# Performance work log

Hardware: AMD Instinct MI355X
Metric: run time of the kernel (lower is better)

Reference implementation:

```python
import jax, jax.numpy as jnp
import numpy as np
import math
from jax import lax

D = 256      # d_model
H = 8        # heads
DK = D // H  # 32
P = 16       # patch size
IMG = 224
S = (IMG // P) ** 2 + 1  # 197
B = 64
EPS = 1e-5


def _ln(x, g, b):
    m = jnp.mean(x, axis=-1, keepdims=True)
    v = jnp.mean((x - m) ** 2, axis=-1, keepdims=True)
    return (x - m) / jnp.sqrt(v + EPS) * g + b


def _attn(q_in, k_in, v_in, wq, bq, wk, bk, wv, bv, wo, bo, mask):
    # torch Linear: y = x @ W^T + b
    def heads(x, w, b):
        y = x @ w.T + b
        bsz, s, _ = y.shape
        return y.reshape(bsz, s, H, DK).transpose(0, 2, 1, 3)  # [b,h,s,dk]
    q = heads(q_in, wq, bq)
    k = heads(k_in, wk, bk)
    v = heads(v_in, wv, bv)
    att = jnp.einsum('bhqd,bhkd->bhqk', q, k) / math.sqrt(DK)
    if mask is not None:
        att = jnp.where(mask == 0, -jnp.inf, att)
    att = jax.nn.softmax(att, axis=-1)
    o = jnp.einsum('bhqk,bhkd->bhqd', att, v)
    bsz, s, _ = q_in.shape  # output reshape uses q's shape (faithful to source)
    o = o.transpose(0, 2, 1, 3).reshape(bsz, s, D)
    return o @ wo.T + bo


def _patch_embed(img, conv_w, conv_b, cls, pos):
    x = lax.conv_general_dilated(img, conv_w, window_strides=(P, P),
                                 padding='VALID',
                                 dimension_numbers=('NCHW', 'OIHW', 'NCHW'))
    x = x + conv_b[None, :, None, None]
    bsz = img.shape[0]
    x = x.reshape(bsz, D, -1).transpose(0, 2, 1)  # [B,196,D]
    cls_t = jnp.broadcast_to(cls, (bsz, 1, D))
    x = jnp.concatenate([x, cls_t], axis=1)  # cls appended at END (faithful)
    return x + pos


def setup_inputs() -> dict:
    key = jax.random.key(0)
    ks = iter(jax.random.split(key, 64))
    nrm = lambda shape, s=0.02: jax.random.normal(next(ks), shape, jnp.float32) * s
    inp = {
        'enc_out': jax.random.normal(next(ks), (B, 3, IMG, IMG), jnp.float32),
        'dec_in': jax.random.normal(next(ks), (B, S, D), jnp.float32),
        'mask': jnp.ones((1, 1, S, S), jnp.int32),
        'conv_w': nrm((D, 3, P, P)),
        'conv_b': jnp.zeros((D,), jnp.float32),
        'cls': nrm((1, 1, D), 1.0),
        'pos': nrm((1, S, D), 1.0),
        'ff_w1': nrm((4 * D, D)), 'ff_b1': jnp.zeros((4 * D,), jnp.float32),
        'ff_w2': nrm((D, 4 * D)), 'ff_b2': jnp.zeros((D,), jnp.float32),
        'ln1_g': jnp.ones((D,), jnp.float32), 'ln1_b': jnp.zeros((D,), jnp.float32),
        'ln2_g': jnp.ones((D,), jnp.float32), 'ln2_b': jnp.zeros((D,), jnp.float32),
        'ln3_g': jnp.ones((D,), jnp.float32), 'ln3_b': jnp.zeros((D,), jnp.float32),
    }
    for p in ('a1', 'a2'):
        for n in ('wq', 'wk', 'wv', 'wo'):
            inp[f'{p}_{n}'] = nrm((D, D))
            inp[f'{p}_b{n[1]}'] = jnp.zeros((D,), jnp.float32)
    return inp


def reference(enc_out, dec_in, mask, conv_w, conv_b, cls, pos,
              ff_w1, ff_b1, ff_w2, ff_b2,
              ln1_g, ln1_b, ln2_g, ln2_b, ln3_g, ln3_b,
              a1_wq, a1_bq, a1_wk, a1_bk, a1_wv, a1_bv, a1_wo, a1_bo,
              a2_wq, a2_bq, a2_wk, a2_bk, a2_wv, a2_bv, a2_wo, a2_bo):
    e = _patch_embed(enc_out, conv_w, conv_b, cls, pos)  # [B,197,D]
    x = dec_in
    x = _ln(x + _attn(dec_in, dec_in, dec_in,
                      a1_wq, a1_bq, a1_wk, a1_bk, a1_wv, a1_bv, a1_wo, a1_bo,
                      None), ln1_g, ln1_b)
    # faithful: q=k=enc_out, v=dec_in, with mask
    x = _ln(x + _attn(e, e, dec_in,
                      a2_wq, a2_bq, a2_wk, a2_bk, a2_wv, a2_bv, a2_wo, a2_bo,
                      mask), ln2_g, ln2_b)
    ff = jax.nn.relu(x @ ff_w1.T + ff_b1) @ ff_w2.T + ff_b2
    x = _ln(x + ff, ln3_g, ln3_b)
    return x
```

## Files before the change

kernel.cpp:

```cpp
#include <hip/hip_runtime.h>
#include <hip/hip_bf16.h>
#include <math.h>

#define DMODEL 256
#define NH 8
#define DKH 32
#define SEQ 197
#define BATCH 64
#define NPAT 196
#define FFDIM 1024
#define KCONV 768
#define EPSLN 1e-5f
#define MROWS (BATCH * SEQ)
#define SP 224

typedef __attribute__((ext_vector_type(8))) short short8;
typedef __attribute__((ext_vector_type(4))) short short4v;
typedef __attribute__((ext_vector_type(4))) float floatx4;

__device__ inline short f2b(float f) {
  unsigned u = __float_as_uint(f);
  unsigned r = (u + 0x7FFFu + ((u >> 16) & 1u)) >> 16;
  return (short)r;
}
__device__ inline float b2f(short s) {
  return __uint_as_float(((unsigned)(unsigned short)s) << 16);
}

typedef const __attribute__((address_space(1))) unsigned int gu32;
typedef __attribute__((address_space(3))) unsigned int lu32;
__device__ __forceinline__ void gl_lds16(const void* g, void* l) {
  __builtin_amdgcn_global_load_lds((gu32*)g, (lu32*)l, 16, 0, 0);
}

__device__ __forceinline__ void gemm64_body(
    char* smem, int bx, int by,
    const short* __restrict__ A, const short* __restrict__ W,
    const float* __restrict__ bias, const short* __restrict__ resb,
    float* __restrict__ outf, short* __restrict__ outb,
    int N, int K, int relu)
{
  short* Al = (short*)smem;
  short* Bl = (short*)(smem + 16384);
  const int t = threadIdx.x;
  const int wave = t >> 6, lane = t & 63;
  const int wm = (wave & 1) * 32, wn = (wave >> 1) * 32;
  const int ml = lane & 15, quad = lane >> 4;
  const int m7 = ml & 7;
  const int m0 = bx * 64, n0 = by * 64;

  const int rs = t >> 3;
  const int cs = (t & 7) ^ (rs & 7);
  const short* gA0 = A + (size_t)(m0 + rs) * K + cs * 8;
  const short* gA1 = A + (size_t)(m0 + rs + 32) * K + cs * 8;
  const short* gB0 = W + (size_t)(n0 + rs) * K + cs * 8;
  const short* gB1 = W + (size_t)(n0 + rs + 32) * K + cs * 8;

  int offA[2][2], offB[2][2];
#pragma unroll
  for (int kk = 0; kk < 2; kk++)
#pragma unroll
    for (int i = 0; i < 2; i++) {
      int ra = wm + i * 16 + ml;
      offA[kk][i] = ra * 64 + (((kk * 4 + quad) ^ m7) * 8);
      int rb = wn + i * 16 + ml;
      offB[kk][i] = rb * 64 + (((kk * 4 + quad) ^ m7) * 8);
    }

  floatx4 z = {0.f, 0.f, 0.f, 0.f};
  floatx4 acc[2][2] = {{z, z}, {z, z}};

  const int niter = K >> 6;
  gl_lds16(gA0, Al + t * 8);
  gl_lds16(gA1, Al + t * 8 + 2048);
  gl_lds16(gB0, Bl + t * 8);
  gl_lds16(gB1, Bl + t * 8 + 2048);
  for (int k = 0; k < niter; k++) {
    int cur = k & 1;
    if (k + 1 < niter) {
      int nb = (cur ^ 1) * 4096;
      int k0 = (k + 1) << 6;
      gl_lds16(gA0 + k0, Al + nb + t * 8);
      gl_lds16(gA1 + k0, Al + nb + t * 8 + 2048);
      gl_lds16(gB0 + k0, Bl + nb + t * 8);
      gl_lds16(gB1 + k0, Bl + nb + t * 8 + 2048);
      __builtin_amdgcn_s_waitcnt(0x0F74);
    } else {
      __builtin_amdgcn_s_waitcnt(0x0F70);
    }
    __asm__ volatile("s_barrier" ::: "memory");
    const short* Ac = Al + cur * 4096;
    const short* Bc = Bl + cur * 4096;
#pragma unroll
    for (int kk = 0; kk < 2; kk++) {
      short8 a0 = *(const short8*)&Ac[offA[kk][0]];
      short8 a1 = *(const short8*)&Ac[offA[kk][1]];
      short8 b0 = *(const short8*)&Bc[offB[kk][0]];
      short8 b1 = *(const short8*)&Bc[offB[kk][1]];
      acc[0][0] = __builtin_amdgcn_mfma_f32_16x16x32_bf16(a0, b0, acc[0][0], 0, 0, 0);
      acc[0][1] = __builtin_amdgcn_mfma_f32_16x16x32_bf16(a0, b1, acc[0][1], 0, 0, 0);
      acc[1][0] = __builtin_amdgcn_mfma_f32_16x16x32_bf16(a1, b0, acc[1][0], 0, 0, 0);
      acc[1][1] = __builtin_amdgcn_mfma_f32_16x16x32_bf16(a1, b1, acc[1][1], 0, 0, 0);
    }
    __asm__ volatile("s_barrier" ::: "memory");
  }
#pragma unroll
  for (int i = 0; i < 2; i++)
#pragma unroll
    for (int j = 0; j < 2; j++)
#pragma unroll
      for (int rr = 0; rr < 4; rr++) {
        int row = m0 + wm + i * 16 + quad * 4 + rr;
        int col = n0 + wn + j * 16 + ml;
        float v = acc[i][j][rr] + bias[col];
        if (resb) v += b2f(resb[(size_t)row * N + col]);
        if (relu) v = fmaxf(v, 0.f);
        if (outf) outf[(size_t)row * N + col] = v;
        if (outb) outb[(size_t)row * N + col] = f2b(v);
      }
}

__device__ __forceinline__ void gemm_full_body(
    char* smem, int bx,
    const short* __restrict__ A, const short* __restrict__ W,
    const float* __restrict__ bias, const short* __restrict__ resb,
    const float* __restrict__ g, const float* __restrict__ bln,
    short* __restrict__ outb, float* __restrict__ outfin, int K)
{
  short* Al = (short*)smem;
  short* Bl = (short*)(smem + 8192);
  const int t = threadIdx.x;
  const int wave = t >> 6, lane = t & 63;
  const int ml = lane & 15, quad = lane >> 4;
  const int m0 = bx * 64;

  const int rs = t >> 2;
  const int cs = (t & 3) ^ ((rs ^ (rs >> 2)) & 3);
  const short* gA = A + (size_t)(m0 + rs) * K + cs * 8;
  const short* gB[4];
#pragma unroll
  for (int j = 0; j < 4; j++)
    gB[j] = W + (size_t)(j * 64 + rs) * K + cs * 8;

  const int sm = (ml ^ (ml >> 2)) & 3;
  const int offA = (wave * 16 + ml) * 32 + ((quad ^ sm) * 8);
  const int offBb = ml * 32 + ((quad ^ sm) * 8);

  floatx4 zv = {0.f, 0.f, 0.f, 0.f};
  floatx4 acc[16];
#pragma unroll
  for (int jj = 0; jj < 16; jj++) acc[jj] = zv;

  const int niter = K >> 5;
  gl_lds16(gA, Al + t * 8);
#pragma unroll
  for (int j = 0; j < 4; j++) gl_lds16(gB[j], Bl + j * 2048 + t * 8);
  for (int k = 0; k < niter; k++) {
    int cur = k & 1;
    if (k + 1 < niter) {
      int k0 = (k + 1) << 5;
      int nbA = (cur ^ 1) * 2048, nbB = (cur ^ 1) * 8192;
      gl_lds16(gA + k0, Al + nbA + t * 8);
#pragma unroll
      for (int j = 0; j < 4; j++) gl_lds16(gB[j] + k0, Bl + nbB + j * 2048 + t * 8);
      __builtin_amdgcn_s_waitcnt(0x0F75);
    } else {
      __builtin_amdgcn_s_waitcnt(0x0F70);
    }
    __asm__ volatile("s_barrier" ::: "memory");
    const short* Ac = Al + cur * 2048;
    const short* Bc = Bl + cur * 8192;
    short8 a = *(const short8*)&Ac[offA];
#pragma unroll
    for (int jj = 0; jj < 16; jj++) {
      short8 b = *(const short8*)&Bc[offBb + jj * 512];
      acc[jj] = __builtin_amdgcn_mfma_f32_16x16x32_bf16(a, b, acc[jj], 0, 0, 0);
    }
    __asm__ volatile("s_barrier" ::: "memory");
  }

  const int rbase = m0 + wave * 16 + quad * 4;
  float bias_r[16], g_r[16], bl_r[16];
#pragma unroll
  for (int jj = 0; jj < 16; jj++) {
    int c = jj * 16 + ml;
    bias_r[jj] = bias[c];
    g_r[jj] = g[c];
    bl_r[jj] = bln[c];
  }
#pragma unroll
  for (int jj = 0; jj < 16; jj++)
#pragma unroll
    for (int rr = 0; rr < 4; rr++)
      acc[jj][rr] += bias_r[jj] + b2f(resb[(size_t)(rbase + rr) * DMODEL + jj * 16 + ml]);
#pragma unroll
  for (int rr = 0; rr < 4; rr++) {
    float s = 0.f;
#pragma unroll
    for (int jj = 0; jj < 16; jj++) s += acc[jj][rr];
    s += __shfl_xor(s, 1); s += __shfl_xor(s, 2);
    s += __shfl_xor(s, 4); s += __shfl_xor(s, 8);
    float mean = s * (1.0f / DMODEL);
    float vs = 0.f;
#pragma unroll
    for (int jj = 0; jj < 16; jj++) {
      float d = acc[jj][rr] - mean;
      vs += d * d;
    }
    vs += __shfl_xor(vs, 1); vs += __shfl_xor(vs, 2);
    vs += __shfl_xor(vs, 4); vs += __shfl_xor(vs, 8);
    float inv = rsqrtf(vs * (1.0f / DMODEL) + EPSLN);
    int row = rbase + rr;
#pragma unroll
    for (int jj = 0; jj < 16; jj++) {
      float o = (acc[jj][rr] - mean) * inv * g_r[jj] + bl_r[jj];
      int col = jj * 16 + ml;
      if (outb) outb[(size_t)row * DMODEL + col] = f2b(o);
      if (outfin) outfin[(size_t)row * DMODEL + col] = o;
    }
  }
}

__device__ __forceinline__ void conv64_body(
    char* smem, int bx, int by,
    const float* __restrict__ img, const short* __restrict__ W,
    const float* __restrict__ cb, const float* __restrict__ pos,
    short* __restrict__ e)
{
  short* Al = (short*)smem;
  short* Bl = (short*)(smem + 8192);
  const int t = threadIdx.x;
  const int wave = t >> 6, lane = t & 63;
  const int wm = (wave & 1) * 32, wn = (wave >> 1) * 32;
  const int ml = lane & 15, quad = lane >> 4;
  const int m7 = ml & 7;
  const int m0 = bx * 64, n0 = by * 64;

  int rA = t >> 3, cg = t & 7;
  int pr_off = cg >> 1;
  int px_off = (cg & 1) * 8;
  int csw = cg ^ (rA & 7);
  const float* baseA[2];
  short* lA[2];
#pragma unroll
  for (int p = 0; p < 2; p++) {
    int m = m0 + rA + p * 32;
    int b = m / NPAT, pp = m - b * NPAT;
    int py = pp / 14, px = pp - py * 14;
    baseA[p] = img + (size_t)b * 3 * 50176 + (size_t)(py * 16) * 224 + px * 16 + px_off;
    lA[p] = &Al[(rA + p * 32) * 64 + csw * 8];
  }
  int rs = t >> 3;
  int cs = (t & 7) ^ (rs & 7);
  const short* gB0 = W + (size_t)(n0 + rs) * KCONV + cs * 8;
  const short* gB1 = W + (size_t)(n0 + rs + 32) * KCONV + cs * 8;

  int offA[2][2], offB[2][2];
#pragma unroll
  for (int kk = 0; kk < 2; kk++)
#pragma unroll
    for (int i = 0; i < 2; i++) {
      int ra = wm + i * 16 + ml;
      offA[kk][i] = ra * 64 + (((kk * 4 + quad) ^ m7) * 8);
      int rb = wn + i * 16 + ml;
      offB[kk][i] = rb * 64 + (((kk * 4 + quad) ^ m7) * 8);
    }

  floatx4 z = {0.f, 0.f, 0.f, 0.f};
  floatx4 acc[2][2] = {{z, z}, {z, z}};

  for (int k0 = 0; k0 < KCONV; k0 += 64) {
    int ch = k0 >> 8;
    int rr0 = (k0 & 255) >> 4;
    __syncthreads();
    gl_lds16(gB0 + k0, Bl + t * 8);
    gl_lds16(gB1 + k0, Bl + t * 8 + 2048);
#pragma unroll
    for (int p = 0; p < 2; p++) {
      const float* ap = baseA[p] + (size_t)ch * 50176 + (rr0 + pr_off) * 224;
      float4 a0 = *(const float4*)ap;
      float4 a1 = *(const float4*)(ap + 4);
      short8 av;
      av[0] = f2b(a0.x); av[1] = f2b(a0.y); av[2] = f2b(a0.z); av[3] = f2b(a0.w);
      av[4] = f2b(a1.x); av[5] = f2b(a1.y); av[6] = f2b(a1.z); av[7] = f2b(a1.w);
      *(short8*)lA[p] = av;
    }
    __builtin_amdgcn_s_waitcnt(0x0F70);
    __syncthreads();
#pragma unroll
    for (int kk = 0; kk < 2; kk++) {
      short8 a0 = *(const short8*)&Al[offA[kk][0]];
      short8 a1 = *(const short8*)&Al[offA[kk][1]];
      short8 b0 = *(const short8*)&Bl[offB[kk][0]];
      short8 b1 = *(const short8*)&Bl[offB[kk][1]];
      acc[0][0] = __builtin_amdgcn_mfma_f32_16x16x32_bf16(a0, b0, acc[0][0], 0, 0, 0);
      acc[0][1] = __builtin_amdgcn_mfma_f32_16x16x32_bf16(a0, b1, acc[0][1], 0, 0, 0);
      acc[1][0] = __builtin_amdgcn_mfma_f32_16x16x32_bf16(a1, b0, acc[1][0], 0, 0, 0);
      acc[1][1] = __builtin_amdgcn_mfma_f32_16x16x32_bf16(a1, b1, acc[1][1], 0, 0, 0);
    }
  }
#pragma unroll
  for (int i = 0; i < 2; i++)
#pragma unroll
    for (int j = 0; j < 2; j++)
#pragma unroll
      for (int rr = 0; rr < 4; rr++) {
        int mrow = m0 + wm + i * 16 + quad * 4 + rr;
        int b2 = mrow / NPAT, p2 = mrow - b2 * NPAT;
        int col = n0 + wn + j * 16 + ml;
        e[((size_t)b2 * SEQ + p2) * DMODEL + col] =
            f2b(acc[i][j][rr] + cb[col] + pos[p2 * DMODEL + col]);
      }
}

__device__ __forceinline__ void attn_body(
    char* smem, int bh,
    const short* __restrict__ qp, int qstr,
    const short* __restrict__ kp, int kstr,
    const short* __restrict__ vp, int vstr,
    const unsigned long long* __restrict__ mbits,
    short* __restrict__ op)
{
  short (*ks)[40] = (short(*)[40])smem;
  short (*vt)[SP + 8] = (short(*)[SP + 8])(smem + 17920);
  short* psw = (short*)(smem + 32768);
  int b = bh >> 3, h = bh & 7;
  int t = threadIdx.x;
  int wave = t >> 6, lane = t & 63;
  int ml = lane & 15, quad = lane >> 4;
  short* ps = psw + wave * 640;

  const short* kb = kp + (size_t)b * SEQ * kstr + h * DKH;
  const short* vb = vp + (size_t)b * SEQ * vstr + h * DKH;
  for (int idx = t; idx < SEQ * 4; idx += 256) {
    int s = idx >> 2, c = (idx & 3) * 8;
    *(short8*)&ks[s][c] = *(const short8*)(kb + (size_t)s * kstr + c);
  }
  for (int idx = t; idx < 1024; idx += 256) {
    int s = ((idx >> 8) << 6) + (idx & 63);
    int c = ((idx >> 6) & 3) * 8;
    if (s < SEQ) {
      short8 v8 = *(const short8*)(vb + (size_t)s * vstr + c);
#pragma unroll
      for (int j = 0; j < 8; j++) vt[c + j][s] = v8[j];
    }
  }
  for (int idx = t; idx < DKH * (SP - SEQ); idx += 256) {
    int d = idx / (SP - SEQ), j = SEQ + idx - d * (SP - SEQ);
    vt[d][j] = 0;
  }
  __syncthreads();

  const float scale = 0.17677669529663687f;
  floatx4 z = {0.f, 0.f, 0.f, 0.f};

  for (int ti = wave; ti < 13; ti += 4) {
    int q0 = ti * 16;
    int qrow = q0 + ml;
    int qc = qrow < SEQ ? qrow : SEQ - 1;
    short8 qf = *(const short8*)(qp + ((size_t)b * SEQ + qc) * qstr + h * DKH + quad * 8);
    const unsigned long long* mrow = mbits + (size_t)qc * 4;

    floatx4 accO0 = z, accO1 = z;
    float mrun = -1e30f, lrun = 0.f;

    for (int st = 0; st < 7; st++) {
      int j0 = st * 32;
      short8 k0 = *(const short8*)&ks[j0 + ml][quad * 8];
      short8 k1 = *(const short8*)&ks[j0 + 16 + ml][quad * 8];
      floatx4 s0 = __builtin_amdgcn_mfma_f32_16x16x32_bf16(k0, qf, z, 0, 0, 0);
      floatx4 s1 = __builtin_amdgcn_mfma_f32_16x16x32_bf16(k1, qf, z, 0, 0, 0);
      unsigned long long mb = mrow[j0 >> 6] >> (j0 & 63);
      float sv[8];
#pragma unroll
      for (int r = 0; r < 4; r++) {
        int jl = quad * 4 + r;
        sv[r]     = ((mb >> jl) & 1ull)        ? s0[r] * scale : -1e38f;
        sv[4 + r] = ((mb >> (16 + jl)) & 1ull) ? s1[r] * scale : -1e38f;
      }
      float tm = sv[0];
#pragma unroll
      for (int i = 1; i < 8; i++) tm = fmaxf(tm, sv[i]);
      tm = fmaxf(tm, __shfl_xor(tm, 16));
      tm = fmaxf(tm, __shfl_xor(tm, 32));
      float nm = fmaxf(mrun, tm);
      float alpha = __expf(mrun - nm);
      float pv[8];
      float psum = 0.f;
#pragma unroll
      for (int i = 0; i < 8; i++) { pv[i] = __expf(sv[i] - nm); psum += pv[i]; }
      psum += __shfl_xor(psum, 16);
      psum += __shfl_xor(psum, 32);
      lrun = lrun * alpha + psum;
      mrun = nm;
      accO0 = accO0 * alpha;
      accO1 = accO1 * alpha;
      short4v p0, p1;
#pragma unroll
      for (int r = 0; r < 4; r++) { p0[r] = f2b(pv[r]); p1[r] = f2b(pv[4 + r]); }
      *(short4v*)&ps[ml * 40 + quad * 4]      = p0;
      *(short4v*)&ps[ml * 40 + 16 + quad * 4] = p1;
      __asm__ volatile("s_waitcnt lgkmcnt(0)" ::: "memory");
      short8 pf = *(const short8*)&ps[ml * 40 + quad * 8];
      short8 vf0 = *(const short8*)&vt[ml][j0 + quad * 8];
      short8 vf1 = *(const short8*)&vt[16 + ml][j0 + quad * 8];
      accO0 = __builtin_amdgcn_mfma_f32_16x16x32_bf16(vf0, pf, accO0, 0, 0, 0);
      accO1 = __builtin_amdgcn_mfma_f32_16x16x32_bf16(vf1, pf, accO1, 0, 0, 0);
    }
    if (qrow < SEQ) {
      float inv = 1.f / lrun;
      short* ob = op + ((size_t)b * SEQ + qrow) * DMODEL + h * DKH;
      short4v o0, o1;
#pragma unroll
      for (int r = 0; r < 4; r++) {
        o0[r] = f2b(accO0[r] * inv);
        o1[r] = f2b(accO1[r] * inv);
      }
      *(short4v*)(ob + quad * 4)      = o0;
      *(short4v*)(ob + 16 + quad * 4) = o1;
    }
  }
}

__global__ __launch_bounds__(256) void phase0(
    const float* wq1, const float* wk1, const float* wv1,
    const float* bq1, const float* bk1, const float* bv1,
    const float* wq2, const float* wk2, const float* bq2, const float* bk2,
    const float* wv2s, const float* wo1, const float* wo2,
    const float* ffw1, const float* ffw2, const float* convw,
    short* Wqkv1, float* Bqkv1, short* Wqk2, float* Bqk2,
    short* Wv2, short* Wo1, short* Wo2, short* Wff1, short* Wff2, short* Wconv,
    const int* mask, unsigned long long* bits, unsigned long long* ones,
    const float* cls, const float* pos, short* e,
    const float* dec, short* dec_bf)
{
  int bid = blockIdx.x;
  int t = threadIdx.x;
  if (bid < 1024) {
    int i = bid * 256 + t;
    if (i < 65536) {
      Wqkv1[i] = f2b(wq1[i]); Wqkv1[65536 + i] = f2b(wk1[i]); Wqkv1[131072 + i] = f2b(wv1[i]);
      Wqk2[i] = f2b(wq2[i]);  Wqk2[65536 + i] = f2b(wk2[i]);
      Wv2[i] = f2b(wv2s[i]);  Wo1[i] = f2b(wo1[i]);  Wo2[i] = f2b(wo2[i]);
    }
    Wff1[i] = f2b(ffw1[i]); Wff2[i] = f2b(ffw2[i]);
    if (i < 196608) Wconv[i] = f2b(convw[i]);
    if (i < 256) {
      Bqkv1[i] = bq1[i]; Bqkv1[256 + i] = bk1[i]; Bqkv1[512 + i] = bv1[i];
      Bqk2[i] = bq2[i];  Bqk2[256 + i] = bk2[i];
    }
  } else if (bid < 1028) {
    int idx = (bid - 1024) * 256 + t;
    if (idx < SEQ * 4) {
      int r = idx >> 2, w = idx & 3;
      unsigned long long bb = 0ull, oo = 0ull;
      for (int j = 0; j < 64; j++) {
        int c = w * 64 + j;
        if (c < SEQ) {
          oo |= (1ull << j);
          if (mask[r * SEQ + c] != 0) bb |= (1ull << j);
        }
      }
      bits[idx] = bb;
      ones[idx] = oo;
    }
  } else if (bid < 1092) {
    int b = bid - 1028, d = t;
    e[((size_t)b * SEQ + NPAT) * DMODEL + d] = f2b(cls[d] + pos[NPAT * DMODEL + d]);
  } else {
    const int ND = (MROWS * DMODEL) / 8;
    int i = (bid - 1092) * 256 + t;
    if (i < ND) {
      float4 a0 = ((const float4*)dec)[i * 2];
      float4 a1 = ((const float4*)dec)[i * 2 + 1];
      short8 o;
      o[0] = f2b(a0.x); o[1] = f2b(a0.y); o[2] = f2b(a0.z); o[3] = f2b(a0.w);
      o[4] = f2b(a1.x); o[5] = f2b(a1.y); o[6] = f2b(a1.z); o[7] = f2b(a1.w);
      ((short8*)dec_bf)[i] = o;
    }
  }
}

__global__ __launch_bounds__(256) void phase1(
    const float* __restrict__ enc, const short* __restrict__ Wconv,
    const float* __restrict__ conv_b, const float* __restrict__ pos,
    short* __restrict__ e_bf,
    const short* __restrict__ dec_bf,
    const short* __restrict__ Wqkv1, const float* __restrict__ Bqkv1,
    short* __restrict__ qkv1,
    const short* __restrict__ Wv2, const float* __restrict__ bv2,
    short* __restrict__ v2)
{
  __shared__ char smem[32768];
  int bid = blockIdx.x;
  if (bid < 784) {
    conv64_body(smem, bid >> 2, bid & 3, enc, Wconv, conv_b, pos, e_bf);
  } else if (bid < 3148) {
    int idx = bid - 784;
    gemm64_body(smem, idx / 12, idx % 12, dec_bf, Wqkv1, Bqkv1, nullptr,
                nullptr, qkv1, 768, 256, 0);
  } else {
    int idx = bid - 3148;
    gemm64_body(smem, idx >> 2, idx & 3, dec_bf, Wv2, bv2, nullptr,
                nullptr, v2, 256, 256, 0);
  }
}

__global__ __launch_bounds__(256) void phase2(
    const short* __restrict__ qkv1, const unsigned long long* __restrict__ mones,
    short* __restrict__ o1,
    const short* __restrict__ e_bf, const short* __restrict__ Wqk2,
    const float* __restrict__ Bqk2, short* __restrict__ qk2)
{
  __shared__ char smem[37888];
  int bid = blockIdx.x;
  if (bid < 512) {
    attn_body(smem, bid, qkv1, 768, qkv1 + 256, 768, qkv1 + 512, 768, mones, o1);
  } else {
    int idx = bid - 512;
    gemm64_body(smem, idx >> 3, idx & 7, e_bf, Wqk2, Bqk2, nullptr,
                nullptr, qk2, 512, 256, 0);
  }
}

__global__ __launch_bounds__(256) void attn_k(
    const short* __restrict__ qp, int qstr,
    const short* __restrict__ kp, int kstr,
    const short* __restrict__ vp, int vstr,
    const unsigned long long* __restrict__ mbits,
    short* __restrict__ op)
{
  __shared__ char smem[37888];
  attn_body(smem, blockIdx.x, qp, qstr, kp, kstr, vp, vstr, mbits, op);
}

__global__ __launch_bounds__(256) void gemm_full_k(
    const short* __restrict__ A, const short* __restrict__ W,
    const float* __restrict__ bias, const short* __restrict__ resb,
    const float* __restrict__ g, const float* __restrict__ bln,
    short* __restrict__ outb, float* __restrict__ outfin, int K)
{
  __shared__ char smem[40960];
  gemm_full_body(smem, blockIdx.x, A, W, bias, resb, g, bln, outb, outfin, K);
}

__global__ __launch_bounds__(256) void gemm_k(
    const short* __restrict__ A, const short* __restrict__ W,
    const float* __restrict__ bias, const short* __restrict__ resb,
    float* __restrict__ outf, short* __restrict__ outb,
    int N, int K, int relu, int nby)
{
  __shared__ char smem[32768];
  gemm64_body(smem, blockIdx.x / nby, blockIdx.x % nby, A, W, bias, resb,
              outf, outb, N, K, relu);
}

extern "C" void kernel_launch(void* const* d_in, const int* in_sizes, int n_in,
                              void* d_out, int out_size, void* d_ws, size_t ws_size,
                              hipStream_t stream)
{
  const float* enc    = (const float*)d_in[0];
  const float* dec_in = (const float*)d_in[1];
  const int*   mask   = (const int*)  d_in[2];
  const float* conv_w = (const float*)d_in[3];
  const float* conv_b = (const float*)d_in[4];
  const float* cls    = (const float*)d_in[5];
  const float* pos    = (const float*)d_in[6];
  const float* ff_w1  = (const float*)d_in[7];
  const float* ff_b1  = (const float*)d_in[8];
  const float* ff_w2  = (const float*)d_in[9];
  const float* ff_b2  = (const float*)d_in[10];
  const float* ln1_g  = (const float*)d_in[11];
  const float* ln1_b  = (const float*)d_in[12];
  const float* ln2_g  = (const float*)d_in[13];
  const float* ln2_b  = (const float*)d_in[14];
  const float* ln3_g  = (const float*)d_in[15];
  const float* ln3_b  = (const float*)d_in[16];
  const float* a1_wq = (const float*)d_in[17]; const float* a1_bq = (const float*)d_in[18];
  const float* a1_wk = (const float*)d_in[19]; const float* a1_bk = (const float*)d_in[20];
  const float* a1_wv = (const float*)d_in[21]; const float* a1_bv = (const float*)d_in[22];
  const float* a1_wo = (const float*)d_in[23]; const float* a1_bo = (const float*)d_in[24];
  const float* a2_wq = (const float*)d_in[25]; const float* a2_bq = (const float*)d_in[26];
  const float* a2_wk = (const float*)d_in[27]; const float* a2_bk = (const float*)d_in[28];
  const float* a2_wv = (const float*)d_in[29]; const float* a2_bv = (const float*)d_in[30];
  const float* a2_wo = (const float*)d_in[31]; const float* a2_bo = (const float*)d_in[32];

  char* wsB = (char*)d_ws;
  short* Wqkv1 = (short*)wsB;
  short* Wqk2  = Wqkv1 + 196608;
  short* Wv2   = Wqk2 + 131072;
  short* Wo1   = Wv2 + 65536;
  short* Wo2   = Wo1 + 65536;
  short* Wff1  = Wo2 + 65536;
  short* Wff2  = Wff1 + 262144;
  short* Wconv = Wff2 + 262144;
  float* Bqkv1 = (float*)(Wconv + 196608);
  float* Bqk2  = Bqkv1 + 768;
  unsigned long long* mbits = (unsigned long long*)(Bqk2 + 512);
  unsigned long long* mones = mbits + 788;

  const size_t MB = 1048576;
  short* dec_bf = (short*)(wsB + 3 * MB);
  short* e_bf   = (short*)(wsB + 10 * MB);
  short* qkv1   = (short*)(wsB + 17 * MB);
  short* o1     = (short*)(wsB + 37 * MB);
  short* qk2    = (short*)(wsB + 44 * MB);
  short* v2     = (short*)(wsB + 57 * MB);
  short* h_buf  = (short*)(wsB + 64 * MB);
  short* x1b    = (short*)(wsB + 97 * MB);
  short* x2b    = (short*)(wsB + 104 * MB);
  short* o2     = o1;

  dim3 blk(256);

  phase0<<<2668, blk, 0, stream>>>(
      a1_wq, a1_wk, a1_wv, a1_bq, a1_bk, a1_bv,
      a2_wq, a2_wk, a2_bq, a2_bk, a2_wv, a1_wo, a2_wo,
      ff_w1, ff_w2, conv_w,
      Wqkv1, Bqkv1, Wqk2, Bqk2, Wv2, Wo1, Wo2, Wff1, Wff2, Wconv,
      mask, mbits, mones, cls, pos, e_bf, dec_in, dec_bf);

  phase1<<<3936, blk, 0, stream>>>(
      enc, Wconv, conv_b, pos, e_bf,
      dec_bf, Wqkv1, Bqkv1, qkv1, Wv2, a2_bv, v2);

  phase2<<<2088, blk, 0, stream>>>(
      qkv1, mones, o1, e_bf, Wqk2, Bqk2, qk2);

  gemm_full_k<<<197, blk, 0, stream>>>(
      o1, Wo1, a1_bo, dec_bf, ln1_g, ln1_b, x1b, nullptr, 256);

  attn_k<<<512, blk, 0, stream>>>(
      qk2, 512, qk2 + 256, 512, v2, 256, mbits, o2);

  gemm_full_k<<<197, blk, 0, stream>>>(
      o2, Wo2, a2_bo, x1b, ln2_g, ln2_b, x2b, nullptr, 256);

  gemm_k<<<3152, blk, 0, stream>>>(
      x2b, Wff1, ff_b1, nullptr, nullptr, h_buf, FFDIM, 256, 1, 16);

  gemm_full_k<<<197, blk, 0, stream>>>(
      h_buf, Wff2, ff_b2, x2b, ln3_g, ln3_b, nullptr, (float*)d_out, 1024);
}
```

Baseline: 326.8 us.

## Keep A row-tile resident in LDS and sweep all output columns per block

Replaces the 64x64 tiled GEMM (grid over M and N tiles) with a row-resident variant: each block loads a 64x256 A tile into LDS once and loops over all N column blocks, streaming only weight slices. The attention-1 QKV and attention-2 V projections are merged into one 1024-wide weight, and the patch-embedding conv computes a full 64x256 output per block. The aim is to avoid re-reading A from global memory for every column tile and to cut block count. In exchange, grids are much smaller (197/393/709 blocks, which may under-fill the GPU), each block runs a long serial loop, and LDS use per block grows.

```diff
diff --git a/kernel.cpp b/kernel.cpp
--- a/kernel.cpp
+++ b/kernel.cpp
@@ -33,91 +33,91 @@
   __builtin_amdgcn_global_load_lds((gu32*)g, (lu32*)l, 16, 0, 0);
 }
 
-__device__ __forceinline__ void gemm64_body(
-    char* smem, int bx, int by,
+__device__ __forceinline__ void gemm_res_body(
+    char* smem, int bx,
     const short* __restrict__ A, const short* __restrict__ W,
-    const float* __restrict__ bias, const short* __restrict__ resb,
-    float* __restrict__ outf, short* __restrict__ outb,
-    int N, int K, int relu)
-{
-  short* Al = (short*)smem;
-  short* Bl = (short*)(smem + 16384);
+    const float* __restrict__ bias,
+    short* __restrict__ outb, int nby, int relu)
+{
+  short* Ar = (short*)smem;
+  short* Bl = (short*)(smem + 33792);
   const int t = threadIdx.x;
   const int wave = t >> 6, lane = t & 63;
   const int wm = (wave & 1) * 32, wn = (wave >> 1) * 32;
   const int ml = lane & 15, quad = lane >> 4;
-  const int m7 = ml & 7;
-  const int m0 = bx * 64, n0 = by * 64;
-
-  const int rs = t >> 3;
-  const int cs = (t & 7) ^ (rs & 7);
-  const short* gA0 = A + (size_t)(m0 + rs) * K + cs * 8;
-  const short* gA1 = A + (size_t)(m0 + rs + 32) * K + cs * 8;
-  const short* gB0 = W + (size_t)(n0 + rs) * K + cs * 8;
-  const short* gB1 = W + (size_t)(n0 + rs + 32) * K + cs * 8;
-
-  int offA[2][2], offB[2][2];
-#pragma unroll
-  for (int kk = 0; kk < 2; kk++)
-#pragma unroll
-    for (int i = 0; i < 2; i++) {
-      int ra = wm + i * 16 + ml;
-      offA[kk][i] = ra * 64 + (((kk * 4 + quad) ^ m7) * 8);
-      int rb = wn + i * 16 + ml;
-      offB[kk][i] = rb * 64 + (((kk * 4 + quad) ^ m7) * 8);
-    }
+  const int m0 = bx * 64;
+  const int Nout = nby * 64;
+
+  {
+    int r = t >> 2, seg = t & 3;
+    const short* gsrc = A + (size_t)(m0 + r) * 256 + seg * 64;
+    short* dst = &Ar[r * 264 + seg * 64];
+#pragma unroll
+    for (int c = 0; c < 8; c++)
+      *(short8*)(dst + c * 8) = *(const short8*)(gsrc + c * 8);
+  }
+  const int rs = t >> 2;
+  const int cs = (t & 3) ^ ((rs ^ (rs >> 2)) & 3);
+  const short* gB = W + (size_t)rs * 256 + cs * 8;
+  short* lB = Bl + t * 8;
+
+  const int rowA0 = (wm + ml) * 264;
+  const int rowA1 = (wm + 16 + ml) * 264;
+  int offB[2];
+#pragma unroll
+  for (int j = 0; j < 2; j++) {
+    int rb = wn + j * 16 + ml;
+    offB[j] = rb * 32 + ((quad ^ ((rb ^ (rb >> 2)) & 3)) * 8);
+  }
+
+  __syncthreads();
 
   floatx4 z = {0.f, 0.f, 0.f, 0.f};
   floatx4 acc[2][2] = {{z, z}, {z, z}};
 
-  const int niter = K >> 6;
-  gl_lds16(gA0, Al + t * 8);
-  gl_lds16(gA1, Al + t * 8 + 2048);
-  gl_lds16(gB0, Bl + t * 8);
-  gl_lds16(gB1, Bl + t * 8 + 2048);
-  for (int k = 0; k < niter; k++) {
-    int cur = k & 1;
-    if (k + 1 < niter) {
-      int nb = (cur ^ 1) * 4096;
-      int k0 = (k + 1) << 6;
-      gl_lds16(gA0 + k0, Al + nb + t * 8);
-      gl_lds16(gA1 + k0, Al + nb + t * 8 + 2048);
-      gl_lds16(gB0 + k0, Bl + nb + t * 8);
-      gl_lds16(gB1 + k0, Bl + nb + t * 8 + 2048);
-      __builtin_amdgcn_s_waitcnt(0x0F74);
+  const int nsteps = nby * 8;
+  gl_lds16(gB, lB);
+  for (int s = 0; s < nsteps; s++) {
+    int by = s >> 3, k = s & 7;
+    if (s + 1 < nsteps) {
+      int by1 = (s + 1) >> 3, k1 = (s + 1) & 7;
+      gl_lds16(gB + (size_t)by1 * (64 * 256) + k1 * 32, lB + ((s + 1) & 1) * 2048);
+      __builtin_amdgcn_s_waitcnt(0x0F71);
     } else {
       __builtin_amdgcn_s_waitcnt(0x0F70);
     }
     __asm__ volatile("s_barrier" ::: "memory");
-    const short* Ac = Al + cur * 4096;
-    const short* Bc = Bl + cur * 4096;
-#pragma unroll
-    for (int kk = 0; kk < 2; kk++) {
-      short8 a0 = *(const short8*)&Ac[offA[kk][0]];
-      short8 a1 = *(const short8*)&Ac[offA[kk][1]];
-      short8 b0 = *(const short8*)&Bc[offB[kk][0]];
-      short8 b1 = *(const short8*)&Bc[offB[kk][1]];
-      acc[0][0] = __builtin_amdgcn_mfma_f32_16x16x32_bf16(a0, b0, acc[0][0], 0, 0, 0);
-      acc[0][1] = __builtin_amdgcn_mfma_f32_16x16x32_bf16(a0, b1, acc[0][1], 0, 0, 0);
-      acc[1][0] = __builtin_amdgcn_mfma_f32_16x16x32_bf16(a1, b0, acc[1][0], 0, 0, 0);
-      acc[1][1] = __builtin_amdgcn_mfma_f32_16x16x32_bf16(a1, b1, acc[1][1], 0, 0, 0);
-    }
+    const short* Bc = Bl + (s & 1) * 2048;
+    int ca = (k * 4 + quad) * 8;
+    short8 a0 = *(const short8*)&Ar[rowA0 + ca];
+    short8 a1 = *(const short8*)&Ar[rowA1 + ca];
+    short8 b0 = *(const short8*)&Bc[offB[0]];
+    short8 b1 = *(const short8*)&Bc[offB[1]];
+    acc[0][0] = __builtin_amdgcn_mfma_f32_16x16x32_bf16(a0, b0, acc[0][0], 0, 0, 0);
+    acc[0][1] = __builtin_amdgcn_mfma_f32_16x16x32_bf16(a0, b1, acc[0][1], 0, 0, 0);
+    acc[1][0] = __builtin_amdgcn_mfma_f32_16x16x32_bf16(a1, b0, acc[1][0], 0, 0, 0);
+    acc[1][1] = __builtin_amdgcn_mfma_f32_16x16x32_bf16(a1, b1, acc[1][1], 0, 0, 0);
     __asm__ volatile("s_barrier" ::: "memory");
-  }
-#pragma unroll
-  for (int i = 0; i < 2; i++)
-#pragma unroll
-    for (int j = 0; j < 2; j++)
-#pragma unroll
-      for (int rr = 0; rr < 4; rr++) {
-        int row = m0 + wm + i * 16 + quad * 4 + rr;
-        int col = n0 + wn + j * 16 + ml;
-        float v = acc[i][j][rr] + bias[col];
-        if (resb) v += b2f(resb[(size_t)row * N + col]);
-        if (relu) v = fmaxf(v, 0.f);
-        if (outf) outf[(size_t)row * N + col] = v;
-        if (outb) outb[(size_t)row * N + col] = f2b(v);
-      }
+    if (k == 7) {
+      int colb = by * 64;
+#pragma unroll
+      for (int i = 0; i < 2; i++)
+#pragma unroll
+        for (int j = 0; j < 2; j++)
+#pragma unroll
+          for (int rr = 0; rr < 4; rr++) {
+            int row = m0 + wm + i * 16 + quad * 4 + rr;
+            int col = colb + wn + j * 16 + ml;
+            float v = acc[i][j][rr] + bias[col];
+            if (relu) v = fmaxf(v, 0.f);
+            outb[(size_t)row * Nout + col] = f2b(v);
+          }
+#pragma unroll
+      for (int i = 0; i < 2; i++)
+#pragma unroll
+        for (int j = 0; j < 2; j++) acc[i][j] = z;
+    }
+  }
 }
 
 __device__ __forceinline__ void gemm_full_body(
@@ -221,96 +221,86 @@
   }
 }
 
-__device__ __forceinline__ void conv64_body(
-    char* smem, int bx, int by,
-    const float* __restrict__ img, const short* __restrict__ W,
+__device__ __forceinline__ void conv_full_body(
+    char* smem, int bx,
+    const float* __restrict__ img, const short* __restrict__ Wc,
     const float* __restrict__ cb, const float* __restrict__ pos,
     short* __restrict__ e)
 {
   short* Al = (short*)smem;
-  short* Bl = (short*)(smem + 8192);
+  short* Bl = (short*)(smem + 4096);
   const int t = threadIdx.x;
   const int wave = t >> 6, lane = t & 63;
-  const int wm = (wave & 1) * 32, wn = (wave >> 1) * 32;
   const int ml = lane & 15, quad = lane >> 4;
-  const int m7 = ml & 7;
-  const int m0 = bx * 64, n0 = by * 64;
-
-  int rA = t >> 3, cg = t & 7;
-  int pr_off = cg >> 1;
-  int px_off = (cg & 1) * 8;
-  int csw = cg ^ (rA & 7);
-  const float* baseA[2];
-  short* lA[2];
-#pragma unroll
-  for (int p = 0; p < 2; p++) {
-    int m = m0 + rA + p * 32;
-    int b = m / NPAT, pp = m - b * NPAT;
-    int py = pp / 14, px = pp - py * 14;
-    baseA[p] = img + (size_t)b * 3 * 50176 + (size_t)(py * 16) * 224 + px * 16 + px_off;
-    lA[p] = &Al[(rA + p * 32) * 64 + csw * 8];
-  }
-  int rs = t >> 3;
-  int cs = (t & 7) ^ (rs & 7);
-  const short* gB0 = W + (size_t)(n0 + rs) * KCONV + cs * 8;
-  const short* gB1 = W + (size_t)(n0 + rs + 32) * KCONV + cs * 8;
-
-  int offA[2][2], offB[2][2];
-#pragma unroll
-  for (int kk = 0; kk < 2; kk++)
-#pragma unroll
-    for (int i = 0; i < 2; i++) {
-      int ra = wm + i * 16 + ml;
-      offA[kk][i] = ra * 64 + (((kk * 4 + quad) ^ m7) * 8);
-      int rb = wn + i * 16 + ml;
-      offB[kk][i] = rb * 64 + (((kk * 4 + quad) ^ m7) * 8);
-    }
-
-  floatx4 z = {0.f, 0.f, 0.f, 0.f};
-  floatx4 acc[2][2] = {{z, z}, {z, z}};
-
-  for (int k0 = 0; k0 < KCONV; k0 += 64) {
-    int ch = k0 >> 8;
-    int rr0 = (k0 & 255) >> 4;
-    __syncthreads();
-    gl_lds16(gB0 + k0, Bl + t * 8);
-    gl_lds16(gB1 + k0, Bl + t * 8 + 2048);
-#pragma unroll
-    for (int p = 0; p < 2; p++) {
-      const float* ap = baseA[p] + (size_t)ch * 50176 + (rr0 + pr_off) * 224;
-      float4 a0 = *(const float4*)ap;
-      float4 a1 = *(const float4*)(ap + 4);
-      short8 av;
-      av[0] = f2b(a0.x); av[1] = f2b(a0.y); av[2] = f2b(a0.z); av[3] = f2b(a0.w);
-      av[4] = f2b(a1.x); av[5] = f2b(a1.y); av[6] = f2b(a1.z); av[7] = f2b(a1.w);
-      *(short8*)lA[p] = av;
-    }
-    __builtin_amdgcn_s_waitcnt(0x0F70);
-    __syncthreads();
-#pragma unroll
-    for (int kk = 0; kk < 2; kk++) {
-      short8 a0 = *(const short8*)&Al[offA[kk][0]];
-      short8 a1 = *(const short8*)&Al[offA[kk][1]];
-      short8 b0 = *(const short8*)&Bl[offB[kk][0]];
-      short8 b1 = *(const short8*)&Bl[offB[kk][1]];
-      acc[0][0] = __builtin_amdgcn_mfma_f32_16x16x32_bf16(a0, b0, acc[0][0], 0, 0, 0);
-      acc[0][1] = __builtin_amdgcn_mfma_f32_16x16x32_bf16(a0, b1, acc[0][1], 0, 0, 0);
-      acc[1][0] = __builtin_amdgcn_mfma_f32_16x16x32_bf16(a1, b0, acc[1][0], 0, 0, 0);
-      acc[1][1] = __builtin_amdgcn_mfma_f32_16x16x32_bf16(a1, b1, acc[1][1], 0, 0, 0);
-    }
-  }
-#pragma unroll
-  for (int i = 0; i < 2; i++)
-#pragma unroll
-    for (int j = 0; j < 2; j++)
-#pragma unroll
-      for (int rr = 0; rr < 4; rr++) {
-        int mrow = m0 + wm + i * 16 + quad * 4 + rr;
-        int b2 = mrow / NPAT, p2 = mrow - b2 * NPAT;
-        int col = n0 + wn + j * 16 + ml;
-        e[((size_t)b2 * SEQ + p2) * DMODEL + col] =
-            f2b(acc[i][j][rr] + cb[col] + pos[p2 * DMODEL + col]);
-      }
+  const int m0 = bx * 64;
+
+  const int r = t >> 2, c = t & 3;
+  const int pr = c >> 1, px8 = (c & 1) * 8;
+  const int csw = c ^ ((r ^ (r >> 2)) & 3);
+  int m = m0 + r;
+  int b = m / NPAT, pp = m - b * NPAT;
+  int py = pp / 14, px = pp - py * 14;
+  const float* gA = img + (size_t)b * 3 * 50176 + (size_t)(py * 16) * 224 + px * 16 + px8;
+  short* lA = &Al[r * 32 + csw * 8];
+
+  const int rs = t >> 2;
+  const int csb = (t & 3) ^ ((rs ^ (rs >> 2)) & 3);
+  const short* gB[4];
+#pragma unroll
+  for (int j = 0; j < 4; j++)
+    gB[j] = Wc + (size_t)(j * 64 + rs) * KCONV + csb * 8;
+
+  const int sm = (ml ^ (ml >> 2)) & 3;
+  const int offA = (wave * 16 + ml) * 32 + ((quad ^ sm) * 8);
+  const int offBb = ml * 32 + ((quad ^ sm) * 8);
+
+  floatx4 zv = {0.f, 0.f, 0.f, 0.f};
+  floatx4 acc[16];
+#pragma unroll
+  for (int jj = 0; jj < 16; jj++) acc[jj] = zv;
+
+  float4 a0 = *(const float4*)gA;
+  float4 a1 = *(const float4*)(gA + 4);
+
+  for (int ks = 0; ks < 24; ks++) {
+    __asm__ volatile("s_barrier" ::: "memory");
+#pragma unroll
+    for (int j = 0; j < 4; j++)
+      gl_lds16(gB[j] + ks * 32, Bl + j * 2048 + t * 8);
+    short8 av;
+    av[0] = f2b(a0.x); av[1] = f2b(a0.y); av[2] = f2b(a0.z); av[3] = f2b(a0.w);
+    av[4] = f2b(a1.x); av[5] = f2b(a1.y); av[6] = f2b(a1.z); av[7] = f2b(a1.w);
+    *(short8*)lA = av;
+    if (ks + 1 < 24) {
+      int ch = (ks + 1) >> 3;
+      int rr2 = ((ks + 1) & 7) * 2 + pr;
+      const float* ap = gA + (size_t)ch * 50176 + rr2 * 224;
+      a0 = *(const float4*)ap;
+      a1 = *(const float4*)(ap + 4);
+    }
+    __builtin_amdgcn_s_waitcnt(0x0072);
+    __asm__ volatile("s_barrier" ::: "memory");
+    short8 a = *(const short8*)&Al[offA];
+#pragma unroll
+    for (int jj = 0; jj < 16; jj++) {
+      short8 bfr = *(const short8*)&Bl[offBb + jj * 512];
+      acc[jj] = __builtin_amdgcn_mfma_f32_16x16x32_bf16(a, bfr, acc[jj], 0, 0, 0);
+    }
+  }
+  __asm__ volatile("s_barrier" ::: "memory");
+
+  const int rb0 = wave * 16 + quad * 4;
+#pragma unroll
+  for (int rr = 0; rr < 4; rr++) {
+    int mrow = m0 + rb0 + rr;
+    int b2 = mrow / NPAT, p2 = mrow - b2 * NPAT;
+    size_t ebase = ((size_t)b2 * SEQ + p2) * DMODEL;
+#pragma unroll
+    for (int jj = 0; jj < 16; jj++) {
+      int col = jj * 16 + ml;
+      e[ebase + col] = f2b(acc[jj][rr] + cb[col] + pos[p2 * DMODEL + col]);
+    }
+  }
 }
 
 __device__ __forceinline__ void attn_body(
@@ -426,10 +416,10 @@
     const float* wq1, const float* wk1, const float* wv1,
     const float* bq1, const float* bk1, const float* bv1,
     const float* wq2, const float* wk2, const float* bq2, const float* bk2,
-    const float* wv2s, const float* wo1, const float* wo2,
+    const float* wv2s, const float* bv2, const float* wo1, const float* wo2,
     const float* ffw1, const float* ffw2, const float* convw,
-    short* Wqkv1, float* Bqkv1, short* Wqk2, float* Bqk2,
-    short* Wv2, short* Wo1, short* Wo2, short* Wff1, short* Wff2, short* Wconv,
+    short* Wqkvv, float* Bqkvv, short* Wqk2, float* Bqk2,
+    short* Wo1, short* Wo2, short* Wff1, short* Wff2, short* Wconv,
     const int* mask, unsigned long long* bits, unsigned long long* ones,
     const float* cls, const float* pos, short* e,
     const float* dec, short* dec_bf)
@@ -439,14 +429,16 @@
   if (bid < 1024) {
     int i = bid * 256 + t;
     if (i < 65536) {
-      Wqkv1[i] = f2b(wq1[i]); Wqkv1[65536 + i] = f2b(wk1[i]); Wqkv1[131072 + i] = f2b(wv1[i]);
+      Wqkvv[i] = f2b(wq1[i]); Wqkvv[65536 + i] = f2b(wk1[i]);
+      Wqkvv[131072 + i] = f2b(wv1[i]); Wqkvv[196608 + i] = f2b(wv2s[i]);
       Wqk2[i] = f2b(wq2[i]);  Wqk2[65536 + i] = f2b(wk2[i]);
-      Wv2[i] = f2b(wv2s[i]);  Wo1[i] = f2b(wo1[i]);  Wo2[i] = f2b(wo2[i]);
+      Wo1[i] = f2b(wo1[i]);  Wo2[i] = f2b(wo2[i]);
     }
     Wff1[i] = f2b(ffw1[i]); Wff2[i] = f2b(ffw2[i]);
     if (i < 196608) Wconv[i] = f2b(convw[i]);
     if (i < 256) {
-      Bqkv1[i] = bq1[i]; Bqkv1[256 + i] = bk1[i]; Bqkv1[512 + i] = bv1[i];
+      Bqkvv[i] = bq1[i]; Bqkvv[256 + i] = bk1[i];
+      Bqkvv[512 + i] = bv1[i]; Bqkvv[768 + i] = bv2[i];
       Bqk2[i] = bq2[i];  Bqk2[256 + i] = bk2[i];
     }
   } else if (bid < 1028) {
@@ -486,40 +478,30 @@
     const float* __restrict__ conv_b, const float* __restrict__ pos,
     short* __restrict__ e_bf,
     const short* __restrict__ dec_bf,
-    const short* __restrict__ Wqkv1, const float* __restrict__ Bqkv1,
-    short* __restrict__ qkv1,
-    const short* __restrict__ Wv2, const float* __restrict__ bv2,
-    short* __restrict__ v2)
-{
-  __shared__ char smem[32768];
+    const short* __restrict__ Wqkvv, const float* __restrict__ Bqkvv,
+    short* __restrict__ qkvv)
+{
+  __shared__ char smem[41984];
   int bid = blockIdx.x;
-  if (bid < 784) {
-    conv64_body(smem, bid >> 2, bid & 3, enc, Wconv, conv_b, pos, e_bf);
-  } else if (bid < 3148) {
-    int idx = bid - 784;
-    gemm64_body(smem, idx / 12, idx % 12, dec_bf, Wqkv1, Bqkv1, nullptr,
-                nullptr, qkv1, 768, 256, 0);
+  if (bid < 196) {
+    conv_full_body(smem, bid, enc, Wconv, conv_b, pos, e_bf);
   } else {
-    int idx = bid - 3148;
-    gemm64_body(smem, idx >> 2, idx & 3, dec_bf, Wv2, bv2, nullptr,
-                nullptr, v2, 256, 256, 0);
+    gemm_res_body(smem, bid - 196, dec_bf, Wqkvv, Bqkvv, qkvv, 16, 0);
   }
 }
 
 __global__ __launch_bounds__(256) void phase2(
-    const short* __restrict__ qkv1, const unsigned long long* __restrict__ mones,
+    const short* __restrict__ qkvv, const unsigned long long* __restrict__ mones,
     short* __restrict__ o1,
     const short* __restrict__ e_bf, const short* __restrict__ Wqk2,
     const float* __restrict__ Bqk2, short* __restrict__ qk2)
 {
-  __shared__ char smem[37888];
+  __shared__ char smem[41984];
   int bid = blockIdx.x;
   if (bid < 512) {
-    attn_body(smem, bid, qkv1, 768, qkv1 + 256, 768, qkv1 + 512, 768, mones, o1);
+    attn_body(smem, bid, qkvv, 1024, qkvv + 256, 1024, qkvv + 512, 1024, mones, o1);
   } else {
-    int idx = bid - 512;
-    gemm64_body(smem, idx >> 3, idx & 7, e_bf, Wqk2, Bqk2, nullptr,
-                nullptr, qk2, 512, 256, 0);
+    gemm_res_body(smem, bid - 512, e_bf, Wqk2, Bqk2, qk2, 8, 0);
   }
 }
 
@@ -544,15 +526,12 @@
   gemm_full_body(smem, blockIdx.x, A, W, bias, resb, g, bln, outb, outfin, K);
 }
 
-__global__ __launch_bounds__(256) void gemm_k(
+__global__ __launch_bounds__(256) void gemm_res_k(
     const short* __restrict__ A, const short* __restrict__ W,
-    const float* __restrict__ bias, const short* __restrict__ resb,
-    float* __restrict__ outf, short* __restrict__ outb,
-    int N, int K, int relu, int nby)
-{
-  __shared__ char smem[32768];
-  gemm64_body(smem, blockIdx.x / nby, blockIdx.x % nby, A, W, bias, resb,
-              outf, outb, N, K, relu);
+    const float* __restrict__ bias, short* __restrict__ outb, int nby, int relu)
+{
+  __shared__ char smem[41984];
+  gemm_res_body(smem, blockIdx.x, A, W, bias, outb, nby, relu);
 }
 
 extern "C" void kernel_launch(void* const* d_in, const int* in_sizes, int n_in,
@@ -586,58 +565,55 @@
   const float* a2_wo = (const float*)d_in[31]; const float* a2_bo = (const float*)d_in[32];
 
   char* wsB = (char*)d_ws;
-  short* Wqkv1 = (short*)wsB;
-  short* Wqk2  = Wqkv1 + 196608;
-  short* Wv2   = Wqk2 + 131072;
-  short* Wo1   = Wv2 + 65536;
+  short* Wqkvv = (short*)wsB;
+  short* Wqk2  = Wqkvv + 262144;
+  short* Wo1   = Wqk2 + 131072;
   short* Wo2   = Wo1 + 65536;
   short* Wff1  = Wo2 + 65536;
   short* Wff2  = Wff1 + 262144;
   short* Wconv = Wff2 + 262144;
-  float* Bqkv1 = (float*)(Wconv + 196608);
-  float* Bqk2  = Bqkv1 + 768;
+  float* Bqkvv = (float*)(Wconv + 196608);
+  float* Bqk2  = Bqkvv + 1024;
   unsigned long long* mbits = (unsigned long long*)(Bqk2 + 512);
   unsigned long long* mones = mbits + 788;
 
   const size_t MB = 1048576;
   short* dec_bf = (short*)(wsB + 3 * MB);
   short* e_bf   = (short*)(wsB + 10 * MB);
-  short* qkv1   = (short*)(wsB + 17 * MB);
-  short* o1     = (short*)(wsB + 37 * MB);
-  short* qk2    = (short*)(wsB + 44 * MB);
-  short* v2     = (short*)(wsB + 57 * MB);
-  short* h_buf  = (short*)(wsB + 64 * MB);
-  short* x1b    = (short*)(wsB + 97 * MB);
-  short* x2b    = (short*)(wsB + 104 * MB);
+  short* qkvv   = (short*)(wsB + 17 * MB);
+  short* o1     = (short*)(wsB + 43 * MB);
+  short* qk2    = (short*)(wsB + 50 * MB);
+  short* h_buf  = (short*)(wsB + 63 * MB);
+  short* x1b    = (short*)(wsB + 89 * MB);
+  short* x2b    = (short*)(wsB + 96 * MB);
   short* o2     = o1;
 
   dim3 blk(256);
 
   phase0<<<2668, blk, 0, stream>>>(
       a1_wq, a1_wk, a1_wv, a1_bq, a1_bk, a1_bv,
-      a2_wq, a2_wk, a2_bq, a2_bk, a2_wv, a1_wo, a2_wo,
+      a2_wq, a2_wk, a2_bq, a2_bk, a2_wv, a2_bv, a1_wo, a2_wo,
       ff_w1, ff_w2, conv_w,
-      Wqkv1, Bqkv1, Wqk2, Bqk2, Wv2, Wo1, Wo2, Wff1, Wff2, Wconv,
+      Wqkvv, Bqkvv, Wqk2, Bqk2, Wo1, Wo2, Wff1, Wff2, Wconv,
       mask, mbits, mones, cls, pos, e_bf, dec_in, dec_bf);
 
-  phase1<<<3936, blk, 0, stream>>>(
-      enc, Wconv, conv_b, pos, e_bf,
-      dec_bf, Wqkv1, Bqkv1, qkv1, Wv2, a2_bv, v2);
-
-  phase2<<<2088, blk, 0, stream>>>(
-      qkv1, mones, o1, e_bf, Wqk2, Bqk2, qk2);
+  phase1<<<393, blk, 0, stream>>>(
+      enc, Wconv, conv_b, pos, e_bf, dec_bf, Wqkvv, Bqkvv, qkvv);
+
+  phase2<<<709, blk, 0, stream>>>(
+      qkvv, mones, o1, e_bf, Wqk2, Bqk2, qk2);
 
   gemm_full_k<<<197, blk, 0, stream>>>(
       o1, Wo1, a1_bo, dec_bf, ln1_g, ln1_b, x1b, nullptr, 256);
 
   attn_k<<<512, blk, 0, stream>>>(
-      qk2, 512, qk2 + 256, 512, v2, 256, mbits, o2);
+      qk2, 512, qk2 + 256, 512, qkvv + 768, 1024, mbits, o2);
 
   gemm_full_k<<<197, blk, 0, stream>>>(
       o2, Wo2, a2_bo, x1b, ln2_g, ln2_b, x2b, nullptr, 256);
 
-  gemm_k<<<3152, blk, 0, stream>>>(
-      x2b, Wff1, ff_b1, nullptr, nullptr, h_buf, FFDIM, 256, 1, 16);
+  gemm_res_k<<<197, blk, 0, stream>>>(
+      x2b, Wff1, ff_b1, h_buf, 16, 1);
 
   gemm_full_k<<<197, blk, 0, stream>>>(
       h_buf, Wff2, ff_b2, x2b, ln3_g, ln3_b, nullptr, (float*)d_out, 1024);
```

Result: slower. 364.3 us (+11.5%).
